# Kernel tuning notes

Hardware: AMD Instinct MI355X
Metric: run time of the kernel (lower is better)

## Reference

```python
import jax, jax.numpy as jnp
import numpy as np

STOCH, DETER, HIDDEN, A, EMBED = 30, 200, 200, 6, 1024
T, B = 64, 512
MIN_STD = 0.1
LN_EPS = 1e-3


def _ln(x, s, b):
    m = jnp.mean(x, -1, keepdims=True)
    v = jnp.mean((x - m) ** 2, -1, keepdims=True)
    return (x - m) * jax.lax.rsqrt(v + LN_EPS) * s + b


def _stats(x):
    mean, std = jnp.split(x, 2, -1)
    return mean, jax.nn.softplus(std) + MIN_STD


def setup_inputs() -> dict:
    key = jax.random.key(0)
    ks = jax.random.split(key, 12)
    w = lambda k, shape, s=0.05: jax.random.normal(k, shape, jnp.float32) * s
    return dict(
        embed=w(ks[0], (T, B, EMBED), 1.0),
        action=w(ks[1], (T, B, A), 1.0),
        is_first=jax.random.randint(ks[2], (T, B), 0, 2).astype(jnp.float32),
        noise_prior=w(ks[3], (T, B, STOCH), 1.0),
        noise_post=w(ks[4], (T, B, STOCH), 1.0),
        w_inp=w(ks[5], (STOCH + A, HIDDEN)),
        ln_inp_s=jnp.ones((HIDDEN,)), ln_inp_b=jnp.zeros((HIDDEN,)),
        w_gru=w(ks[6], (HIDDEN + DETER, 3 * DETER)),
        w_imgout=w(ks[7], (DETER, HIDDEN)),
        ln_img_s=jnp.ones((HIDDEN,)), ln_img_b=jnp.zeros((HIDDEN,)),
        w_obsout=w(ks[8], (DETER + EMBED, HIDDEN)),
        ln_obs_s=jnp.ones((HIDDEN,)), ln_obs_b=jnp.zeros((HIDDEN,)),
        w_ims=w(ks[9], (HIDDEN, 2 * STOCH)), b_ims=jnp.zeros((2 * STOCH,)),
        w_obs=w(ks[10], (HIDDEN, 2 * STOCH)), b_obs=jnp.zeros((2 * STOCH,)),
        w_init=w(ks[11], (1, DETER), 0.1),
    )


def reference(embed, action, is_first, noise_prior, noise_post,
              w_inp, ln_inp_s, ln_inp_b, w_gru, w_imgout, ln_img_s, ln_img_b,
              w_obsout, ln_obs_s, ln_obs_b, w_ims, b_ims, w_obs, b_obs, w_init):
    # learned initial state: deter0 = tanh(W), stoch0 = mode (mean) of img stats
    deter0 = jnp.tanh(w_init) * jnp.ones((B, 1), embed.dtype)          # [B, DETER]
    h0 = jax.nn.silu(_ln(deter0 @ w_imgout, ln_img_s, ln_img_b))
    stoch0, _ = _stats(h0 @ w_ims + b_ims)                              # [B, STOCH]

    def step(carry, xs):
        stoch, deter = carry
        a_t, e_t, f_t, nzp, nzq = xs
        # action magnitude clip with stop-gradient scale
        a = a_t * jax.lax.stop_gradient(1.0 / jnp.maximum(jnp.abs(a_t), 1.0))
        f = f_t[:, None]
        a = a * (1.0 - f)
        stoch = stoch * (1.0 - f) + stoch0 * f
        deter = deter * (1.0 - f) + deter0 * f
        # img_step (prior): inp layers -> GRU cell -> img_out -> stats
        x = jax.nn.silu(_ln(jnp.concatenate([stoch, a], -1) @ w_inp, ln_inp_s, ln_inp_b))
        parts = jnp.concatenate([x, deter], -1) @ w_gru                 # [B, 3*DETER]
        r, c, u = jnp.split(parts, 3, -1)
        r = jax.nn.sigmoid(r)
        c = jnp.tanh(r * c)
        u = jax.nn.sigmoid(u - 1.0)                                     # update_bias = -1
        deter = u * c + (1.0 - u) * deter
        hp = jax.nn.silu(_ln(deter @ w_imgout, ln_img_s, ln_img_b))
        pm, ps = _stats(hp @ w_ims + b_ims)
        prior_stoch = pm + ps * nzp                                     # rsample
        # obs_step (posterior, temp_post=True): concat(deter, embed)
        ho = jax.nn.silu(_ln(jnp.concatenate([deter, e_t], -1) @ w_obsout, ln_obs_s, ln_obs_b))
        qm, qs = _stats(ho @ w_obs + b_obs)
        post_stoch = qm + qs * nzq
        out_t = jnp.concatenate([qm, qs, post_stoch, pm, ps, prior_stoch, deter], -1)
        return (post_stoch, deter), out_t

    _, out = jax.lax.scan(step, (stoch0, deter0),
                          (action, embed, is_first, noise_prior, noise_post))
    return out  # [T, B, 6*STOCH + DETER] = post(mean,std,stoch), prior(mean,std,stoch), deter
```

## Files before the change

### kernel.cpp

```cpp
#include <hip/hip_runtime.h>
#include <math.h>

#define T_STEPS 64
#define BATCH   512

typedef short s16x8 __attribute__((ext_vector_type(8)));
typedef float f32x4 __attribute__((ext_vector_type(4)));

#define MFMA(a,b,c) __builtin_amdgcn_mfma_f32_16x16x32_bf16((a),(b),(c),0,0,0)

__device__ __forceinline__ short f2bf(float x){
    union { float f; unsigned u; } v; v.f = x;
    unsigned r = v.u + 0x7FFFu + ((v.u >> 16) & 1u);
    return (short)(r >> 16);
}
__device__ __forceinline__ float bf2f(short s){
    union { unsigned u; float f; } v; v.u = ((unsigned)(unsigned short)s) << 16;
    return v.f;
}
__device__ __forceinline__ float frcp(float x){ return __builtin_amdgcn_rcpf(x); }
__device__ __forceinline__ float fsig(float x){ return frcp(1.f + __expf(-x)); }
__device__ __forceinline__ float ftanh(float x){ return 1.f - 2.f*frcp(1.f + __expf(2.f*x)); }
__device__ __forceinline__ float sp(float x){ return (x>20.f)? x : __logf(1.f + __expf(x)); }

#define FR_GRU   0
#define FR_INP   494
#define FR_OBSD  520
#define FR_OBSE  611
#define FR_OBS   1027
#define FR_IMG   1055
#define FR_IMS   1146
#define FR_TOT   1174

#define WS_STOCH0 1202176
#define WS_DETER0 1202304
#define WS_E      1203200

__global__ void pack_kernel(const float* w_inp, const float* w_gru, const float* w_imgout,
                            const float* w_obsout, const float* w_ims, const float* w_obs,
                            short* pk){
    int f = blockIdx.x, l = threadIdx.x;
    const float* W; int K, N, ld, KT, k0, rel;
    if      (f < FR_INP ){ W=w_gru;    K=400; N=600; ld=600; KT=13; k0=0;   rel=f; }
    else if (f < FR_OBSD){ W=w_inp;    K=36;  N=200; ld=200; KT=2;  k0=0;   rel=f-FR_INP; }
    else if (f < FR_OBSE){ W=w_obsout; K=200; N=200; ld=200; KT=7;  k0=0;   rel=f-FR_OBSD; }
    else if (f < FR_OBS ){ W=w_obsout; K=1024;N=200; ld=200; KT=32; k0=200; rel=f-FR_OBSE; }
    else if (f < FR_IMG ){ W=w_obs;    K=200; N=60;  ld=60;  KT=7;  k0=0;   rel=f-FR_OBS; }
    else if (f < FR_IMS ){ W=w_imgout; K=200; N=200; ld=200; KT=7;  k0=0;   rel=f-FR_IMG; }
    else                 { W=w_ims;    K=200; N=60;  ld=60;  KT=7;  k0=0;   rel=f-FR_IMS; }
    int nt = rel / KT, kt = rel % KT;
    int col = nt*16 + (l & 15);
    int kb  = kt*32 + (l >> 4)*8;
    s16x8 v;
    #pragma unroll
    for (int e = 0; e < 8; e++){
        int k = kb + e;
        float x = (k < K && col < N) ? W[(size_t)(k + k0)*ld + col] : 0.f;
        v[e] = f2bf(x);
    }
    *(((s16x8*)pk) + (size_t)f*64 + l) = v;
}

__global__ void init_kernel(const float* w_init, const float* w_imgout,
                            const float* ln_img_s, const float* ln_img_b,
                            const float* w_ims, const float* b_ims,
                            float* stoch0, float* deter0){
    __shared__ float d0[200], h0[200], redA[64], redB[64], mv[2];
    int t = threadIdx.x;
    if (t < 200) d0[t] = tanhf(w_init[t]);
    __syncthreads();
    if (t < 200){ float a = 0.f; for (int k = 0; k < 200; k++) a += d0[k]*w_imgout[k*200 + t]; h0[t] = a; }
    __syncthreads();
    if (t < 64){ float s = 0.f, s2 = 0.f;
        for (int j = t; j < 200; j += 64){ float v = h0[j]; s += v; s2 += v*v; }
        redA[t] = s; redB[t] = s2; }
    __syncthreads();
    if (t == 0){ float s = 0.f, s2 = 0.f;
        for (int i = 0; i < 64; i++){ s += redA[i]; s2 += redB[i]; }
        float m = s/200.f, var = s2/200.f - m*m;
        mv[0] = m; mv[1] = rsqrtf(var + 1e-3f); }
    __syncthreads();
    if (t < 200){ float v = (h0[t]-mv[0])*mv[1]*ln_img_s[t] + ln_img_b[t];
        h0[t] = v/(1.f+expf(-v)); }
    __syncthreads();
    if (t < 200) deter0[t] = d0[t];
    if (t < 30){ float a = 0.f; for (int j = 0; j < 200; j++) a += h0[j]*w_ims[j*60 + t];
        stoch0[t] = a + b_ims[t]; }
}

__global__ __launch_bounds__(256) void embed_gemm(const float* embed, const short* pk, short* E){
    int tid = threadIdx.x; int w = tid >> 6, l = tid & 63;
    int row0 = blockIdx.x*128 + w*32;
    const float* A0 = embed + (size_t)(row0 + (l & 15))*1024 + (l >> 4)*8;
    const float* A1 = A0 + (size_t)16*1024;
    const s16x8* B = ((const s16x8*)pk) + (size_t)FR_OBSE*64 + l;
    f32x4 acc0[13], acc1[13];
    #pragma unroll
    for (int n = 0; n < 13; n++){ acc0[n] = (f32x4){0.f,0.f,0.f,0.f}; acc1[n] = (f32x4){0.f,0.f,0.f,0.f}; }
    for (int kt = 0; kt < 32; kt++){
        float4 x0 = *(const float4*)(A0 + kt*32), x1 = *(const float4*)(A0 + kt*32 + 4);
        float4 y0 = *(const float4*)(A1 + kt*32), y1 = *(const float4*)(A1 + kt*32 + 4);
        s16x8 af0, af1;
        af0[0]=f2bf(x0.x); af0[1]=f2bf(x0.y); af0[2]=f2bf(x0.z); af0[3]=f2bf(x0.w);
        af0[4]=f2bf(x1.x); af0[5]=f2bf(x1.y); af0[6]=f2bf(x1.z); af0[7]=f2bf(x1.w);
        af1[0]=f2bf(y0.x); af1[1]=f2bf(y0.y); af1[2]=f2bf(y0.z); af1[3]=f2bf(y0.w);
        af1[4]=f2bf(y1.x); af1[5]=f2bf(y1.y); af1[6]=f2bf(y1.z); af1[7]=f2bf(y1.w);
        #pragma unroll
        for (int n = 0; n < 13; n++){
            s16x8 bf = B[(n*32 + kt)*64];
            acc0[n] = MFMA(af0, bf, acc0[n]);
            acc1[n] = MFMA(af1, bf, acc1[n]);
        }
    }
    int rr = (l >> 4)*4, cc = l & 15;
    #pragma unroll
    for (int n = 0; n < 13; n++){
        int col = n*16 + cc;
        if (col < 200){
            #pragma unroll
            for (int r = 0; r < 4; r++){
                E[(size_t)(row0 + rr + r)*200 + col]        = f2bf(acc0[n][r]);
                E[(size_t)(row0 + 16 + rr + r)*200 + col]   = f2bf(acc1[n][r]);
            }
        }
    }
}

#define AB_STRIDE 424
#define XP_STRIDE 212
#define PT_STRIDE 612
#define QP_STRIDE 68
#define A36_STRIDE 72
#define HO_STRIDE 224

__global__ __launch_bounds__(512) void scan_kernel(
    const float* action, const float* is_first, const float* noise_post,
    const float* ln_inp_s, const float* ln_inp_b,
    const float* ln_obs_s, const float* ln_obs_b,
    const float* b_obs,
    const short* pk, const short* E, const float* stoch0g, const float* deter0g,
    float* out)
{
    __shared__ short Abuf[16*AB_STRIDE];
    __shared__ float U[16*PT_STRIDE];
    __shared__ short A36hob[16*HO_STRIDE];
    __shared__ float Sbuf[16*30];

    int tid = threadIdx.x;
    int w = tid >> 6, l = tid & 63;
    int row = tid >> 5, s = tid & 31;
    int r0 = blockIdx.x*16;

    float dreg[7];
    #pragma unroll
    for (int i = 0; i < 7; i++){ int j = s + 32*i; dreg[i] = (j < 200) ? deter0g[j] : 0.f; }
    if (s < 30) Sbuf[row*30 + s] = stoch0g[s];
    for (int idx = tid; idx < 16*24; idx += 512){ int rr = idx/24; Abuf[rr*AB_STRIDE + 400 + idx%24] = 0; }

    float lisr[7], libr[7], losr[7], lobr[7];
    #pragma unroll
    for (int i = 0; i < 7; i++){ int j = s + 32*i; bool ok = j < 200;
        lisr[i] = ok ? ln_inp_s[j] : 0.f;  libr[i] = ok ? ln_inp_b[j] : 0.f;
        losr[i] = ok ? ln_obs_s[j] : 0.f;  lobr[i] = ok ? ln_obs_b[j] : 0.f;
    }
    float bo0 = 0.f, bo1 = 0.f;
    if (tid < 480){ int j = tid % 30; bo0 = b_obs[j]; bo1 = b_obs[30 + j]; }

    __syncthreads();

    for (int t = 0; t < T_STEPS; t++){
        float f = is_first[(size_t)t*BATCH + r0 + row];
        #pragma unroll
        for (int i = 0; i < 7; i++){ int j = s + 32*i; if (j < 200){
            float d = dreg[i]*(1.f - f) + deter0g[j]*f;
            dreg[i] = d;
            Abuf[row*AB_STRIDE + 200 + j] = f2bf(d);
        }}
        for (int j = s; j < 64; j += 32){
            float v = 0.f;
            if (j < 30) v = Sbuf[row*30 + j]*(1.f - f) + stoch0g[j]*f;
            else if (j < 36){
                float a = action[(size_t)((size_t)t*BATCH + r0 + row)*6 + (j - 30)];
                a = a * frcp(fmaxf(fabsf(a), 1.f));
                v = a*(1.f - f);
            }
            A36hob[row*A36_STRIDE + j] = f2bf(v);
        }
        s16x8 Ech;
        if (tid < 400){
            int er = tid/25, eq = tid%25;
            Ech = *(((const s16x8*)(E + (size_t)((size_t)t*BATCH + r0 + er)*200)) + eq);
        }
        float nz = 0.f;
        if (tid < 480){
            int rw = tid/30, j = tid%30;
            nz = noise_post[(size_t)((size_t)t*BATCH + r0 + rw)*30 + j];
        }
        __syncthreads();

        {
            s16x8 a0 = *(s16x8*)&A36hob[(l & 15)*A36_STRIDE + (l >> 4)*8];
            s16x8 a1 = *(s16x8*)&A36hob[(l & 15)*A36_STRIDE + 32 + (l >> 4)*8];
            for (int nt = w; nt < 13; nt += 8){
                f32x4 acc = (f32x4){0.f,0.f,0.f,0.f};
                const s16x8* B = ((const s16x8*)pk) + (size_t)(FR_INP + nt*2)*64 + l;
                acc = MFMA(a0, B[0],  acc);
                acc = MFMA(a1, B[64], acc);
                int rr = (l >> 4)*4, cc = l & 15;
                #pragma unroll
                for (int r = 0; r < 4; r++) U[(rr + r)*XP_STRIDE + nt*16 + cc] = acc[r];
            }
        }
        __syncthreads();

        {
            float sum = 0.f, sq = 0.f, vals[7];
            #pragma unroll
            for (int i = 0; i < 7; i++){ int j = s + 32*i;
                float v = (j < 200) ? U[row*XP_STRIDE + j] : 0.f;
                vals[i] = v; sum += v; sq += v*v; }
            #pragma unroll
            for (int m = 16; m >= 1; m >>= 1){ sum += __shfl_xor(sum, m); sq += __shfl_xor(sq, m); }
            float mean = sum/200.f, var = sq/200.f - mean*mean, rstd = rsqrtf(var + 1e-3f);
            #pragma unroll
            for (int i = 0; i < 7; i++){ int j = s + 32*i; if (j < 200){
                float v = (vals[i] - mean)*rstd*lisr[i] + libr[i];
                Abuf[row*AB_STRIDE + j] = f2bf(v*fsig(v));
            }}
        }
        __syncthreads();

        {
            s16x8 af[13];
            #pragma unroll
            for (int kt = 0; kt < 13; kt++)
                af[kt] = *(s16x8*)&Abuf[(l & 15)*AB_STRIDE + kt*32 + (l >> 4)*8];
            for (int nt = w; nt < 38; nt += 8){
                f32x4 acc = (f32x4){0.f,0.f,0.f,0.f};
                const s16x8* B = ((const s16x8*)pk) + (size_t)(FR_GRU + nt*13)*64 + l;
                #pragma unroll
                for (int kt = 0; kt < 13; kt++) acc = MFMA(af[kt], B[kt*64], acc);
                int rr = (l >> 4)*4, cc = l & 15;
                #pragma unroll
                for (int r = 0; r < 4; r++) U[(rr + r)*PT_STRIDE + nt*16 + cc] = acc[r];
            }
        }
        __syncthreads();

        {
            float* outp = out + (size_t)((size_t)t*BATCH + r0 + row)*380;
            #pragma unroll
            for (int i = 0; i < 7; i++){ int j = s + 32*i; if (j < 200){
                float rv = U[row*PT_STRIDE + j];
                float cv = U[row*PT_STRIDE + 200 + j];
                float uv = U[row*PT_STRIDE + 400 + j];
                float rg = fsig(rv);
                float cg = ftanh(rg*cv);
                float ug = fsig(uv - 1.f);
                float d  = ug*cg + (1.f - ug)*dreg[i];
                dreg[i] = d;
                Abuf[row*AB_STRIDE + 200 + j] = f2bf(d);
                outp[180 + j] = d;
            }}
        }
        __syncthreads();

        {
            s16x8 af[7];
            #pragma unroll
            for (int kt = 0; kt < 7; kt++)
                af[kt] = *(s16x8*)&Abuf[(l & 15)*AB_STRIDE + 200 + kt*32 + (l >> 4)*8];
            for (int nt = w; nt < 13; nt += 8){
                f32x4 acc = (f32x4){0.f,0.f,0.f,0.f};
                const s16x8* B = ((const s16x8*)pk) + (size_t)(FR_OBSD + nt*7)*64 + l;
                #pragma unroll
                for (int kt = 0; kt < 7; kt++) acc = MFMA(af[kt], B[kt*64], acc);
                int rr = (l >> 4)*4, cc = l & 15;
                #pragma unroll
                for (int r = 0; r < 4; r++) U[(rr + r)*XP_STRIDE + nt*16 + cc] = acc[r];
            }
        }
        __syncthreads();

        if (tid < 400){
            int er = tid/25, eq = tid%25;
            #pragma unroll
            for (int e = 0; e < 8; e++) U[er*XP_STRIDE + eq*8 + e] += bf2f(Ech[e]);
        }
        __syncthreads();

        {
            float sum = 0.f, sq = 0.f, vals[7];
            #pragma unroll
            for (int i = 0; i < 7; i++){ int j = s + 32*i;
                float v = (j < 200) ? U[row*XP_STRIDE + j] : 0.f;
                vals[i] = v; sum += v; sq += v*v; }
            #pragma unroll
            for (int m = 16; m >= 1; m >>= 1){ sum += __shfl_xor(sum, m); sq += __shfl_xor(sq, m); }
            float mean = sum/200.f, var = sq/200.f - mean*mean, rstd = rsqrtf(var + 1e-3f);
            #pragma unroll
            for (int i = 0; i < 7; i++){ int j = s + 32*i;
                short hv = 0;
                if (j < 200){
                    float v = (vals[i] - mean)*rstd*losr[i] + lobr[i];
                    hv = f2bf(v*fsig(v));
                }
                A36hob[row*HO_STRIDE + j] = hv;
            }
        }
        __syncthreads();

        if (w < 4){
            s16x8 af[7];
            #pragma unroll
            for (int kt = 0; kt < 7; kt++)
                af[kt] = *(s16x8*)&A36hob[(l & 15)*HO_STRIDE + kt*32 + (l >> 4)*8];
            int nt = w;
            f32x4 acc = (f32x4){0.f,0.f,0.f,0.f};
            const s16x8* B = ((const s16x8*)pk) + (size_t)(FR_OBS + nt*7)*64 + l;
            #pragma unroll
            for (int kt = 0; kt < 7; kt++) acc = MFMA(af[kt], B[kt*64], acc);
            int rr = (l >> 4)*4, cc = l & 15;
            #pragma unroll
            for (int r = 0; r < 4; r++) U[(rr + r)*QP_STRIDE + nt*16 + cc] = acc[r];
        }
        __syncthreads();

        if (tid < 480){
            int rw = tid/30, j = tid%30;
            float qm = U[rw*QP_STRIDE + j] + bo0;
            float x  = U[rw*QP_STRIDE + 30 + j] + bo1;
            float qs = sp(x) + 0.1f;
            float post = qm + qs*nz;
            float* outp = out + (size_t)((size_t)t*BATCH + r0 + rw)*380;
            outp[j] = qm; outp[30 + j] = qs; outp[60 + j] = post;
            Sbuf[rw*30 + j] = post;
        }
        __syncthreads();
    }
}

__global__ __launch_bounds__(64) void prior_kernel(const float* noise_prior, const float* b_ims,
                                                   const float* ln_img_s, const float* ln_img_b,
                                                   const short* pk, float* out){
    __shared__ short Ab[16*232];
    __shared__ float U[16*212];
    __shared__ short hob[16*224];
    __shared__ float qp[16*68];
    int l = threadIdx.x;
    int g0 = blockIdx.x*16;

    for (int idx = l; idx < 16*232; idx += 64){
        int rr = idx/232, c = idx%232;
        short v = 0;
        if (c < 200) v = f2bf(out[(size_t)(g0 + rr)*380 + 180 + c]);
        Ab[idx] = v;
    }
    __syncthreads();
    {
        s16x8 af[7];
        #pragma unroll
        for (int kt = 0; kt < 7; kt++)
            af[kt] = *(s16x8*)&Ab[(l & 15)*232 + kt*32 + (l >> 4)*8];
        for (int nt = 0; nt < 13; nt++){
            f32x4 acc = (f32x4){0.f,0.f,0.f,0.f};
            const s16x8* B = ((const s16x8*)pk) + (size_t)(FR_IMG + nt*7)*64 + l;
            #pragma unroll
            for (int kt = 0; kt < 7; kt++) acc = MFMA(af[kt], B[kt*64], acc);
            int rr = (l >> 4)*4, cc = l & 15;
            #pragma unroll
            for (int r = 0; r < 4; r++) U[(rr + r)*212 + nt*16 + cc] = acc[r];
        }
    }
    __syncthreads();
    {
        int rw = l >> 2, s4 = l & 3;
        float sum = 0.f, sq = 0.f, vals[50];
        #pragma unroll
        for (int i = 0; i < 50; i++){ int j = s4 + 4*i; float v = U[rw*212 + j];
            vals[i] = v; sum += v; sq += v*v; }
        sum += __shfl_xor(sum, 1); sq += __shfl_xor(sq, 1);
        sum += __shfl_xor(sum, 2); sq += __shfl_xor(sq, 2);
        float mean = sum/200.f, var = sq/200.f - mean*mean, rstd = rsqrtf(var + 1e-3f);
        #pragma unroll
        for (int i = 0; i < 50; i++){ int j = s4 + 4*i;
            float v = (vals[i] - mean)*rstd*ln_img_s[j] + ln_img_b[j];
            hob[rw*224 + j] = f2bf(v*fsig(v));
        }
    }
    for (int idx = l; idx < 16*24; idx += 64){ int rr = idx/24; hob[rr*224 + 200 + idx%24] = 0; }
    __syncthreads();
    for (int nt = 0; nt < 4; nt++){
        s16x8 af[7];
        #pragma unroll
        for (int kt = 0; kt < 7; kt++)
            af[kt] = *(s16x8*)&hob[(l & 15)*224 + kt*32 + (l >> 4)*8];
        f32x4 acc = (f32x4){0.f,0.f,0.f,0.f};
        const s16x8* B = ((const s16x8*)pk) + (size_t)(FR_IMS + nt*7)*64 + l;
        #pragma unroll
        for (int kt = 0; kt < 7; kt++) acc = MFMA(af[kt], B[kt*64], acc);
        int rr = (l >> 4)*4, cc = l & 15;
        #pragma unroll
        for (int r = 0; r < 4; r++) qp[(rr + r)*68 + nt*16 + cc] = acc[r];
    }
    __syncthreads();
    for (int idx = l; idx < 480; idx += 64){
        int rw = idx/30, j = idx%30;
        float pm = qp[rw*68 + j] + b_ims[j];
        float x  = qp[rw*68 + 30 + j] + b_ims[30 + j];
        float ps = sp(x) + 0.1f;
        float nz = noise_prior[(size_t)(g0 + rw)*30 + j];
        float prior = pm + ps*nz;
        float* op = out + (size_t)(g0 + rw)*380;
        op[90 + j] = pm; op[120 + j] = ps; op[150 + j] = prior;
    }
}

extern "C" void kernel_launch(void* const* d_in, const int* in_sizes, int n_in,
                              void* d_out, int out_size, void* d_ws, size_t ws_size,
                              hipStream_t stream){
    const float* embed    = (const float*)d_in[0];
    const float* action   = (const float*)d_in[1];
    const float* is_first = (const float*)d_in[2];
    const float* nzp      = (const float*)d_in[3];
    const float* nzq      = (const float*)d_in[4];
    const float* w_inp    = (const float*)d_in[5];
    const float* ln_inp_s = (const float*)d_in[6];
    const float* ln_inp_b = (const float*)d_in[7];
    const float* w_gru    = (const float*)d_in[8];
    const float* w_imgout = (const float*)d_in[9];
    const float* ln_img_s = (const float*)d_in[10];
    const float* ln_img_b = (const float*)d_in[11];
    const float* w_obsout = (const float*)d_in[12];
    const float* ln_obs_s = (const float*)d_in[13];
    const float* ln_obs_b = (const float*)d_in[14];
    const float* w_ims    = (const float*)d_in[15];
    const float* b_ims    = (const float*)d_in[16];
    const float* w_obs    = (const float*)d_in[17];
    const float* b_obs    = (const float*)d_in[18];
    const float* w_init   = (const float*)d_in[19];

    char*  ws    = (char*)d_ws;
    short* pk    = (short*)ws;
    float* stoch0 = (float*)(ws + WS_STOCH0);
    float* deter0 = (float*)(ws + WS_DETER0);
    short* E      = (short*)(ws + WS_E);
    float* out    = (float*)d_out;

    hipLaunchKernelGGL(pack_kernel, dim3(FR_TOT), dim3(64), 0, stream,
                       w_inp, w_gru, w_imgout, w_obsout, w_ims, w_obs, pk);
    hipLaunchKernelGGL(init_kernel, dim3(1), dim3(256), 0, stream,
                       w_init, w_imgout, ln_img_s, ln_img_b, w_ims, b_ims, stoch0, deter0);
    hipLaunchKernelGGL(embed_gemm, dim3(256), dim3(256), 0, stream, embed, pk, E);
    hipLaunchKernelGGL(scan_kernel, dim3(32), dim3(512), 0, stream,
                       action, is_first, nzq, ln_inp_s, ln_inp_b, ln_obs_s, ln_obs_b, b_obs,
                       pk, E, stoch0, deter0, out);
    hipLaunchKernelGGL(prior_kernel, dim3(2048), dim3(64), 0, stream, nzp, b_ims, ln_img_s, ln_img_b, pk, out);
}
```

Before: 906.6 us.

## Stage small weights in LDS, prefetch GRU/obs weights, split MFMA accumulators

Copies the input-projection and obs-deter weight fragments into shared memory once per block, so they are no longer reloaded from global memory every timestep. The GRU weight fragments are double-buffered in registers (ga/gb), with the first tile prefetched before the preceding barrier, and the posterior-head weights are prefetched early. MFMA chains are split across two independent accumulators to shorten the dependency chain. GRU pre-activations are stored as bf16 so the shared U buffer shrinks, which adds a rounding step before the gates. The change uses much more LDS and registers, and the launch bound is set to one block per CU.

```diff
diff --git a/kernel.cpp b/kernel.cpp
--- a/kernel.cpp
+++ b/kernel.cpp
@@ -127,13 +127,25 @@
 }
 
 #define AB_STRIDE 424
-#define XP_STRIDE 212
-#define PT_STRIDE 612
+#define XP_STRIDE 210
+#define PB_STRIDE 612
 #define QP_STRIDE 68
 #define A36_STRIDE 72
 #define HO_STRIDE 224
 
-__global__ __launch_bounds__(512) void scan_kernel(
+#define MM2NT(SRC, NT) { \
+    f32x4 p0={0.f,0.f,0.f,0.f}, p1={0.f,0.f,0.f,0.f}; \
+    p0=MFMA(af[0],SRC[0],p0);   p1=MFMA(af[1],SRC[1],p1); \
+    p0=MFMA(af[2],SRC[2],p0);   p1=MFMA(af[3],SRC[3],p1); \
+    p0=MFMA(af[4],SRC[4],p0);   p1=MFMA(af[5],SRC[5],p1); \
+    p0=MFMA(af[6],SRC[6],p0);   p1=MFMA(af[7],SRC[7],p1); \
+    p0=MFMA(af[8],SRC[8],p0);   p1=MFMA(af[9],SRC[9],p1); \
+    p0=MFMA(af[10],SRC[10],p0); p1=MFMA(af[11],SRC[11],p1); \
+    p0=MFMA(af[12],SRC[12],p0); \
+    _Pragma("unroll") \
+    for (int r=0;r<4;r++) Pbs[(rr+r)*PB_STRIDE + (NT)*16 + cc] = f2bf(p0[r]+p1[r]); }
+
+__global__ __launch_bounds__(512,1) void scan_kernel(
     const float* action, const float* is_first, const float* noise_post,
     const float* ln_inp_s, const float* ln_inp_b,
     const float* ln_obs_s, const float* ln_obs_b,
@@ -142,20 +154,34 @@
     float* out)
 {
     __shared__ short Abuf[16*AB_STRIDE];
-    __shared__ float U[16*PT_STRIDE];
+    __shared__ __align__(16) char Uraw[19584];
     __shared__ short A36hob[16*HO_STRIDE];
     __shared__ float Sbuf[16*30];
+    __shared__ short WI[26*512];
+    __shared__ short WD[91*512];
+
+    float* Uf  = (float*)Uraw;
+    short* Pbs = (short*)Uraw;
 
     int tid = threadIdx.x;
     int w = tid >> 6, l = tid & 63;
     int row = tid >> 5, s = tid & 31;
     int r0 = blockIdx.x*16;
+    const int rr = (l >> 4)*4, cc = l & 15;
+    const s16x8* PK = (const s16x8*)pk;
+
+    for (int f = w; f < 26; f += 8)
+        *(s16x8*)&WI[f*512 + l*8] = PK[(size_t)(FR_INP + f)*64 + l];
+    for (int f = w; f < 91; f += 8)
+        *(s16x8*)&WD[f*512 + l*8] = PK[(size_t)(FR_OBSD + f)*64 + l];
 
     float dreg[7];
     #pragma unroll
     for (int i = 0; i < 7; i++){ int j = s + 32*i; dreg[i] = (j < 200) ? deter0g[j] : 0.f; }
     if (s < 30) Sbuf[row*30 + s] = stoch0g[s];
-    for (int idx = tid; idx < 16*24; idx += 512){ int rr = idx/24; Abuf[rr*AB_STRIDE + 400 + idx%24] = 0; }
+    for (int idx = tid; idx < 16*24; idx += 512){ int q = idx/24; Abuf[q*AB_STRIDE + 400 + idx%24] = 0; }
+    #pragma unroll
+    for (int i = 0; i < 7; i++){ int j = s + 32*i; if (j < 200) Abuf[row*AB_STRIDE + 200 + j] = f2bf(dreg[i]); }
 
     float lisr[7], libr[7], losr[7], lobr[7];
     #pragma unroll
@@ -169,6 +195,9 @@
     __syncthreads();
 
     for (int t = 0; t < T_STEPS; t++){
+        s16x8 ga[13], gb[13];
+        s16x8 m4w[7];
+
         float f = is_first[(size_t)t*BATCH + r0 + row];
         #pragma unroll
         for (int i = 0; i < 7; i++){ int j = s + 32*i; if (j < 200){
@@ -203,12 +232,10 @@
             s16x8 a1 = *(s16x8*)&A36hob[(l & 15)*A36_STRIDE + 32 + (l >> 4)*8];
             for (int nt = w; nt < 13; nt += 8){
                 f32x4 acc = (f32x4){0.f,0.f,0.f,0.f};
-                const s16x8* B = ((const s16x8*)pk) + (size_t)(FR_INP + nt*2)*64 + l;
-                acc = MFMA(a0, B[0],  acc);
-                acc = MFMA(a1, B[64], acc);
-                int rr = (l >> 4)*4, cc = l & 15;
+                acc = MFMA(a0, *(const s16x8*)&WI[(nt*2+0)*512 + l*8], acc);
+                acc = MFMA(a1, *(const s16x8*)&WI[(nt*2+1)*512 + l*8], acc);
                 #pragma unroll
-                for (int r = 0; r < 4; r++) U[(rr + r)*XP_STRIDE + nt*16 + cc] = acc[r];
+                for (int r = 0; r < 4; r++) Uf[(rr + r)*XP_STRIDE + nt*16 + cc] = acc[r];
             }
         }
         __syncthreads();
@@ -217,7 +244,7 @@
             float sum = 0.f, sq = 0.f, vals[7];
             #pragma unroll
             for (int i = 0; i < 7; i++){ int j = s + 32*i;
-                float v = (j < 200) ? U[row*XP_STRIDE + j] : 0.f;
+                float v = (j < 200) ? Uf[row*XP_STRIDE + j] : 0.f;
                 vals[i] = v; sum += v; sq += v*v; }
             #pragma unroll
             for (int m = 16; m >= 1; m >>= 1){ sum += __shfl_xor(sum, m); sq += __shfl_xor(sq, m); }
@@ -228,6 +255,11 @@
                 Abuf[row*AB_STRIDE + j] = f2bf(v*fsig(v));
             }}
         }
+        {
+            const s16x8* Bp = PK + (size_t)(FR_GRU + w*13)*64 + l;
+            #pragma unroll
+            for (int kt=0;kt<13;kt++) ga[kt] = Bp[kt*64];
+        }
         __syncthreads();
 
         {
@@ -235,25 +267,48 @@
             #pragma unroll
             for (int kt = 0; kt < 13; kt++)
                 af[kt] = *(s16x8*)&Abuf[(l & 15)*AB_STRIDE + kt*32 + (l >> 4)*8];
-            for (int nt = w; nt < 38; nt += 8){
-                f32x4 acc = (f32x4){0.f,0.f,0.f,0.f};
-                const s16x8* B = ((const s16x8*)pk) + (size_t)(FR_GRU + nt*13)*64 + l;
+            {
+                const s16x8* Bp = PK + (size_t)(FR_GRU + (w+8)*13)*64 + l;
                 #pragma unroll
-                for (int kt = 0; kt < 13; kt++) acc = MFMA(af[kt], B[kt*64], acc);
-                int rr = (l >> 4)*4, cc = l & 15;
+                for (int kt=0;kt<13;kt++) gb[kt] = Bp[kt*64];
+            }
+            MM2NT(ga, w);
+            {
+                const s16x8* Bp = PK + (size_t)(FR_GRU + (w+16)*13)*64 + l;
                 #pragma unroll
-                for (int r = 0; r < 4; r++) U[(rr + r)*PT_STRIDE + nt*16 + cc] = acc[r];
-            }
-        }
-        __syncthreads();
-
+                for (int kt=0;kt<13;kt++) ga[kt] = Bp[kt*64];
+            }
+            MM2NT(gb, w+8);
+            {
+                const s16x8* Bp = PK + (size_t)(FR_GRU + (w+24)*13)*64 + l;
+                #pragma unroll
+                for (int kt=0;kt<13;kt++) gb[kt] = Bp[kt*64];
+            }
+            MM2NT(ga, w+16);
+            if (w < 6){
+                const s16x8* Bp = PK + (size_t)(FR_GRU + (w+32)*13)*64 + l;
+                #pragma unroll
+                for (int kt=0;kt<13;kt++) ga[kt] = Bp[kt*64];
+            }
+            MM2NT(gb, w+24);
+            if (w < 6){
+                MM2NT(ga, w+32);
+            }
+        }
+        __syncthreads();
+
+        if (w < 4){
+            const s16x8* Bp = PK + (size_t)(FR_OBS + w*7)*64 + l;
+            #pragma unroll
+            for (int kt=0;kt<7;kt++) m4w[kt] = Bp[kt*64];
+        }
         {
             float* outp = out + (size_t)((size_t)t*BATCH + r0 + row)*380;
             #pragma unroll
             for (int i = 0; i < 7; i++){ int j = s + 32*i; if (j < 200){
-                float rv = U[row*PT_STRIDE + j];
-                float cv = U[row*PT_STRIDE + 200 + j];
-                float uv = U[row*PT_STRIDE + 400 + j];
+                float rv = bf2f(Pbs[row*PB_STRIDE + j]);
+                float cv = bf2f(Pbs[row*PB_STRIDE + 200 + j]);
+                float uv = bf2f(Pbs[row*PB_STRIDE + 400 + j]);
                 float rg = fsig(rv);
                 float cg = ftanh(rg*cv);
                 float ug = fsig(uv - 1.f);
@@ -266,18 +321,21 @@
         __syncthreads();
 
         {
-            s16x8 af[7];
+            s16x8 ad[7];
             #pragma unroll
             for (int kt = 0; kt < 7; kt++)
-                af[kt] = *(s16x8*)&Abuf[(l & 15)*AB_STRIDE + 200 + kt*32 + (l >> 4)*8];
+                ad[kt] = *(s16x8*)&Abuf[(l & 15)*AB_STRIDE + 200 + kt*32 + (l >> 4)*8];
             for (int nt = w; nt < 13; nt += 8){
-                f32x4 acc = (f32x4){0.f,0.f,0.f,0.f};
-                const s16x8* B = ((const s16x8*)pk) + (size_t)(FR_OBSD + nt*7)*64 + l;
+                f32x4 a0={0.f,0.f,0.f,0.f}, a1={0.f,0.f,0.f,0.f};
+                a0 = MFMA(ad[0], *(const s16x8*)&WD[(nt*7+0)*512 + l*8], a0);
+                a1 = MFMA(ad[1], *(const s16x8*)&WD[(nt*7+1)*512 + l*8], a1);
+                a0 = MFMA(ad[2], *(const s16x8*)&WD[(nt*7+2)*512 + l*8], a0);
+                a1 = MFMA(ad[3], *(const s16x8*)&WD[(nt*7+3)*512 + l*8], a1);
+                a0 = MFMA(ad[4], *(const s16x8*)&WD[(nt*7+4)*512 + l*8], a0);
+                a1 = MFMA(ad[5], *(const s16x8*)&WD[(nt*7+5)*512 + l*8], a1);
+                a0 = MFMA(ad[6], *(const s16x8*)&WD[(nt*7+6)*512 + l*8], a0);
                 #pragma unroll
-                for (int kt = 0; kt < 7; kt++) acc = MFMA(af[kt], B[kt*64], acc);
-                int rr = (l >> 4)*4, cc = l & 15;
-                #pragma unroll
-                for (int r = 0; r < 4; r++) U[(rr + r)*XP_STRIDE + nt*16 + cc] = acc[r];
+                for (int r = 0; r < 4; r++) Uf[(rr + r)*XP_STRIDE + nt*16 + cc] = a0[r]+a1[r];
             }
         }
         __syncthreads();
@@ -285,7 +343,7 @@
         if (tid < 400){
             int er = tid/25, eq = tid%25;
             #pragma unroll
-            for (int e = 0; e < 8; e++) U[er*XP_STRIDE + eq*8 + e] += bf2f(Ech[e]);
+            for (int e = 0; e < 8; e++) Uf[er*XP_STRIDE + eq*8 + e] += bf2f(Ech[e]);
         }
         __syncthreads();
 
@@ -293,7 +351,7 @@
             float sum = 0.f, sq = 0.f, vals[7];
             #pragma unroll
             for (int i = 0; i < 7; i++){ int j = s + 32*i;
-                float v = (j < 200) ? U[row*XP_STRIDE + j] : 0.f;
+                float v = (j < 200) ? Uf[row*XP_STRIDE + j] : 0.f;
                 vals[i] = v; sum += v; sq += v*v; }
             #pragma unroll
             for (int m = 16; m >= 1; m >>= 1){ sum += __shfl_xor(sum, m); sq += __shfl_xor(sq, m); }
@@ -311,25 +369,24 @@
         __syncthreads();
 
         if (w < 4){
-            s16x8 af[7];
+            s16x8 ah[7];
             #pragma unroll
             for (int kt = 0; kt < 7; kt++)
-                af[kt] = *(s16x8*)&A36hob[(l & 15)*HO_STRIDE + kt*32 + (l >> 4)*8];
-            int nt = w;
-            f32x4 acc = (f32x4){0.f,0.f,0.f,0.f};
-            const s16x8* B = ((const s16x8*)pk) + (size_t)(FR_OBS + nt*7)*64 + l;
-            #pragma unroll
-            for (int kt = 0; kt < 7; kt++) acc = MFMA(af[kt], B[kt*64], acc);
-            int rr = (l >> 4)*4, cc = l & 15;
-            #pragma unroll
-            for (int r = 0; r < 4; r++) U[(rr + r)*QP_STRIDE + nt*16 + cc] = acc[r];
+                ah[kt] = *(s16x8*)&A36hob[(l & 15)*HO_STRIDE + kt*32 + (l >> 4)*8];
+            f32x4 a0={0.f,0.f,0.f,0.f}, a1={0.f,0.f,0.f,0.f};
+            a0=MFMA(ah[0],m4w[0],a0); a1=MFMA(ah[1],m4w[1],a1);
+            a0=MFMA(ah[2],m4w[2],a0); a1=MFMA(ah[3],m4w[3],a1);
+            a0=MFMA(ah[4],m4w[4],a0); a1=MFMA(ah[5],m4w[5],a1);
+            a0=MFMA(ah[6],m4w[6],a0);
+            #pragma unroll
+            for (int r = 0; r < 4; r++) Uf[(rr + r)*QP_STRIDE + w*16 + cc] = a0[r]+a1[r];
         }
         __syncthreads();
 
         if (tid < 480){
             int rw = tid/30, j = tid%30;
-            float qm = U[rw*QP_STRIDE + j] + bo0;
-            float x  = U[rw*QP_STRIDE + 30 + j] + bo1;
+            float qm = Uf[rw*QP_STRIDE + j] + bo0;
+            float x  = Uf[rw*QP_STRIDE + 30 + j] + bo1;
             float qs = sp(x) + 0.1f;
             float post = qm + qs*nz;
             float* outp = out + (size_t)((size_t)t*BATCH + r0 + rw)*380;
```

New measurement: 1.316 ms. 1.45x slower.
